# Kernel tuning notes

Hardware: AMD Instinct MI355X
Metric: run time of the kernel (lower is better)

The kernel has to match this reference:

```python
import jax, jax.numpy as jnp
import numpy as np

B, S, D_IN, D_SRC, D_OUT = 128, 2048, 1024, 1024, 1024
W = 64                      # window_size
WL = 2 * W + 1              # window_length
STD_SQ = (W / 2.0) ** 2
EPS = 1e-14


def setup_inputs() -> dict:
    key = jax.random.key(0)
    ks = jax.random.split(key, 8)
    inp = jax.random.normal(ks[0], (B, D_IN), dtype=jnp.float32)
    source_hids = jax.random.normal(ks[1], (S, B, D_SRC), dtype=jnp.float32)
    # per-sample valid lengths; must satisfy L <= S - WL so the dynamic window stays in-bounds
    lengths = jax.random.randint(ks[2], (B,), 1024, S - WL + 1)
    encoder_padding_mask = jnp.arange(S)[:, None] >= lengths[None, :]  # [S, B], True = pad
    d_half = (D_IN + 1) // 2
    u = lambda k, shape, a: jax.random.uniform(k, shape, jnp.float32, -a, a)
    Wi = u(ks[3], (D_SRC, D_IN), 0.1)             # input_proj (no bias)
    Wo = u(ks[4], (D_OUT, D_IN + D_SRC), 0.1)     # output_proj (no bias)
    b1_bound = 1.0 / np.sqrt(D_IN)
    W1 = u(ks[5], (d_half, D_IN), b1_bound); b1 = u(ks[5], (d_half,), b1_bound)
    b2_bound = 1.0 / np.sqrt(d_half)
    W2 = u(ks[6], (1, d_half), b2_bound); b2 = u(ks[6], (1,), b2_bound)
    return {"input": inp, "source_hids": source_hids,
            "encoder_padding_mask": encoder_padding_mask,
            "Wi": Wi, "Wo": Wo, "W1": W1, "b1": b1, "W2": W2, "b2": b2}


def reference(input, source_hids, encoder_padding_mask, Wi, Wo, W1, b1, W2, b2):
    lengths = jnp.sum(~encoder_padding_mask, axis=0).astype(jnp.float32)  # [B]
    x = input @ Wi.T                                                      # [B, D_SRC]
    # predicted window center p = W + L * sigmoid(fc2(tanh(fc1(x))))
    p_sig = jax.nn.sigmoid(jnp.tanh(x @ W1.T + b1) @ W2.T + b2)[:, 0]     # [B]
    p = W + lengths * p_sig                                               # [B]
    window_start = jnp.round(p - W).astype(jnp.int32)                     # [B]
    positions = window_start[:, None].astype(jnp.float32) + jnp.arange(WL, dtype=jnp.float32)  # [B, WL]
    # per-sample dynamic window gather from [B, S, D]
    src_bt = jnp.transpose(source_hids, (1, 0, 2))
    selection = jax.vmap(
        lambda s, st: jax.lax.dynamic_slice(s, (st, 0), (WL, s.shape[1]))
    )(src_bt, window_start)                                               # [B, WL, D_SRC]
    gaussian = jnp.exp(-(positions - p[:, None]) ** 2 / (2.0 * STD_SQ))   # [B, WL]
    score = jnp.einsum('bd,bwd->bw', x, selection)                        # [B, WL]
    # valid absolute positions are [W, L + W); outside -> epsilon (matches torch loop)
    valid = (positions >= W) & (positions < lengths[:, None] + W)
    score = jnp.where(valid, score, EPS)
    a = jax.nn.softmax(score, axis=1) * gaussian                          # [B, WL]
    c = jnp.einsum('bw,bwd->bd', a, selection)                            # [B, D_SRC]
    out = jnp.tanh(jnp.concatenate((c, input), axis=1) @ Wo.T)            # [B, D_OUT]
    return out, a, window_start, window_start + WL
```

## Files before the change

kernel.cpp:

```cpp
#include <hip/hip_runtime.h>
#include <math.h>

#define BB   128
#define SS   2048
#define DIN  1024
#define DSRC 1024
#define DOUT 1024
#define WW   64
#define WLEN 129
#define HH   512
#define WCH  17
#define GW   136

#define OFF_WSI   0
#define OFF_P     512
#define OFF_LEN   1024
#define OFF_GTAB  4096
#define OFF_XP    73728
#define OFF_X32   4268032
#define OFF_Z1P   4792320
#define OFF_C32   6889472
#define OFF_CPART 7413760
#define OFF_MPART 11608064
#define OFF_LPART 11612160
#define OFF_SPART 11616256
#define OFF_OP    11685888
#define WS_NEED   15880192

#define DO_A    (BB*DOUT)
#define DO_WS   (DO_A + BB*WLEN)
#define DO_WE   (DO_WS + BB)

template<int NTOT, int KRANGE, bool F64OUT>
__device__ __forceinline__ void gemm16(const int gblk, const int t,
    const float* __restrict__ A, const int lda,
    const float* __restrict__ Wt, const int ldw,
    void* __restrict__ outp, float* __restrict__ alds )
{
    constexpr int NJB = NTOT / 16;
    const int jb = gblk % NJB;
    const int ks = gblk / NJB;
    const int lane = t & 63;
    const int wvid = __builtin_amdgcn_readfirstlane(t >> 6);
    const int j0 = jb * 16 + wvid * 2;
    const int k0 = ks * KRANGE;

    double dac[2][2];
    dac[0][0] = 0.0; dac[0][1] = 0.0; dac[1][0] = 0.0; dac[1][1] = 0.0;

    const float* wbase = Wt + (size_t)j0 * ldw;

    for (int kc = 0; kc < KRANGE; kc += 64) {
        const int kg = k0 + kc;
        __syncthreads();
        #pragma unroll
        for (int q = 0; q < 4; ++q) {
            const int f4 = t + 512 * q;
            const int bb = f4 >> 4, c4 = f4 & 15;
            const float4 v = *reinterpret_cast<const float4*>(A + (size_t)bb * lda + kg + c4 * 4);
            alds[(c4*4+0)*130 + bb] = v.x;
            alds[(c4*4+1)*130 + bb] = v.y;
            alds[(c4*4+2)*130 + bb] = v.z;
            alds[(c4*4+3)*130 + bb] = v.w;
        }
        __syncthreads();
        const float* wr = wbase + kg;
        #pragma unroll
        for (int kk16 = 0; kk16 < 64; kk16 += 16) {
            float fa[2][2];
            fa[0][0] = 0.f; fa[0][1] = 0.f; fa[1][0] = 0.f; fa[1][1] = 0.f;
            #pragma unroll
            for (int kk = 0; kk < 16; ++kk) {
                const int k = kk16 + kk;
                const float2 av = *reinterpret_cast<const float2*>(&alds[k*130 + 2*lane]);
                #pragma unroll
                for (int jj = 0; jj < 2; ++jj) {
                    const float wvv = wr[jj*ldw + k];
                    fa[jj][0] = fmaf(wvv, av.x, fa[jj][0]);
                    fa[jj][1] = fmaf(wvv, av.y, fa[jj][1]);
                }
            }
            #pragma unroll
            for (int jj = 0; jj < 2; ++jj) {
                dac[jj][0] += (double)fa[jj][0];
                dac[jj][1] += (double)fa[jj][1];
            }
        }
    }
    #pragma unroll
    for (int i = 0; i < 2; ++i) {
        const int b = 2*lane + i;
        const size_t base = ((size_t)ks * BB + b) * NTOT + j0;
        if constexpr (F64OUT) {
            double* o = (double*)outp;
            o[base + 0] = dac[0][i];
            o[base + 1] = dac[1][i];
        } else {
            float* o = (float*)outp;
            o[base + 0] = (float)dac[0][i];
            o[base + 1] = (float)dac[1][i];
        }
    }
}

__global__ __launch_bounds__(512)
void k_combo(const float* __restrict__ input, const float* __restrict__ Wi,
             const float* __restrict__ Wo, const unsigned char* __restrict__ mask,
             double* __restrict__ xp, float* __restrict__ op4, int* __restrict__ lengths)
{
    __shared__ __align__(16) float alds[64*130];
    const int blk = blockIdx.x, t = threadIdx.x;
    if (blk < 256) {
        gemm16<1024, 256, true>(blk, t, input, DIN, Wi, DIN, xp, alds);
    } else if (blk < 512) {
        gemm16<1024, 256, false>(blk - 256, t, input, DIN, Wo + 1024, DIN + DSRC, op4, alds);
    } else {
        const int b = blk - 512;
        const bool is_u8 = (mask[(size_t)SS*BB - 1] != 0);
        int cnt = 0;
        if (is_u8) {
            #pragma unroll
            for (int q = 0; q < 4; ++q)
                cnt += (mask[(size_t)(t + 512*q)*BB + b] != 0) ? 1 : 0;
        } else {
            const int* m32 = (const int*)mask;
            #pragma unroll
            for (int q = 0; q < 4; ++q)
                cnt += (m32[(size_t)(t + 512*q)*BB + b] != 0) ? 1 : 0;
        }
        int* red = (int*)alds;
        red[t] = cnt;
        __syncthreads();
        for (int st = 256; st >= 1; st >>= 1) {
            if (t < st) red[t] += red[t + st];
            __syncthreads();
        }
        if (t == 0) lengths[b] = SS - red[0];
    }
}

__global__ __launch_bounds__(512)
void k_xred(const double* __restrict__ xp, float* __restrict__ x32)
{
    const int i = blockIdx.x * 512 + threadIdx.x;
    double s = 0.0;
    #pragma unroll
    for (int ks = 0; ks < 4; ++ks) s += xp[(size_t)ks * (BB*DSRC) + i];
    x32[i] = (float)s;
}

__global__ __launch_bounds__(512)
void k_fc1(const float* __restrict__ x32, const float* __restrict__ W1, double* __restrict__ z1p)
{
    __shared__ __align__(16) float alds[64*130];
    gemm16<512, 256, true>(blockIdx.x, threadIdx.x, x32, DSRC, W1, DIN, z1p, alds);
}

__global__ __launch_bounds__(64)
void k_fc2(const double* __restrict__ z1p, const float* __restrict__ b1,
           const float* __restrict__ W2f, const float* __restrict__ b2,
           const int* __restrict__ lengths, int* __restrict__ wsi,
           float* __restrict__ pbuf, float* __restrict__ gtab, float* __restrict__ dout)
{
    const int b = blockIdx.x, lane = threadIdx.x;
    double part = 0.0;
    #pragma unroll
    for (int q = 0; q < 8; ++q) {
        const int h = lane + 64*q;
        double z = 0.0;
        #pragma unroll
        for (int ks = 0; ks < 4; ++ks) z += z1p[((size_t)ks*BB + b)*HH + h];
        z += (double)b1[h];
        part += tanh(z) * (double)W2f[h];
    }
    #pragma unroll
    for (int off = 32; off >= 1; off >>= 1) part += __shfl_xor(part, off);
    const double z2  = part + (double)b2[0];
    const double sig = 1.0 / (1.0 + exp(-z2));
    const double wsf = (double)lengths[b] * sig;
    int W0 = (int)rint(wsf);
    if (W0 < 0) W0 = 0;
    if (W0 > SS - WLEN) W0 = SS - WLEN;
    const float pf = (float)(wsf + 64.0);
    if (lane == 0) {
        wsi[b]  = W0;
        pbuf[b] = pf;
        dout[DO_WS + b] = (float)W0;
        dout[DO_WE + b] = (float)(W0 + WLEN);
    }
    #pragma unroll
    for (int q = 0; q < 3; ++q) {
        const int w = lane + 64*q;
        if (w < GW) {
            float g = 0.f;
            if (w < WLEN) {
                const float d = (float)(W0 + w) - pf;
                g = expf(d*d * (-1.0f/2048.0f));
            }
            gtab[b*GW + w] = g;
        }
    }
}

__global__ __launch_bounds__(256)
void k_score(const float* __restrict__ x32, const float* __restrict__ src,
             const int* __restrict__ wsi, const float* __restrict__ pbuf,
             const int* __restrict__ lengths, const float* __restrict__ gtab,
             float* __restrict__ cpart, float* __restrict__ mpart,
             float* __restrict__ lpart, float* __restrict__ spart)
{
    const int wc = blockIdx.x, b = blockIdx.y;
    const int t = threadIdx.x, lane = t & 63, wv = t >> 6;
    const int   w0 = wsi[b];
    const int   L  = lengths[b];

    const float4 x4 = *reinterpret_cast<const float4*>(x32 + b*DSRC + 4*t);

    float4 sel[WCH];
    #pragma unroll
    for (int i = 0; i < WCH; ++i) {
        const int w = wc*WCH + i;
        if (w < WLEN) {
            const size_t off = ((size_t)(w0 + w) * BB + b) * DSRC + 4*t;
            sel[i] = *reinterpret_cast<const float4*>(src + off);
        } else sel[i] = make_float4(0.f, 0.f, 0.f, 0.f);
    }

    float w_[32];
    #pragma unroll
    for (int i = 0; i < WCH; ++i)
        w_[i] = fmaf(x4.x, sel[i].x, fmaf(x4.y, sel[i].y, fmaf(x4.z, sel[i].z, x4.w * sel[i].w)));
    #pragma unroll
    for (int i = WCH; i < 32; ++i) w_[i] = 0.f;

    #pragma unroll
    for (int k = 0; k < 5; ++k) {
        const int dist = 1 << k;
        const bool hi = (lane >> k) & 1;
        const int n2 = 32 >> (k + 1);
        #pragma unroll
        for (int i = 0; i < n2; ++i) {
            const float keep = hi ? w_[2*i+1] : w_[2*i];
            const float send = hi ? w_[2*i]   : w_[2*i+1];
            w_[i] = keep + __shfl_xor(send, dist);
        }
    }
    const float tot = w_[0] + __shfl_xor(w_[0], 32);

    __shared__ float red[WCH][4];
    __shared__ float s_sh[WCH];
    if (lane < WCH) red[lane][wv] = tot;
    __syncthreads();
    if (t < WCH) {
        const int w = wc*WCH + t;
        float s;
        if (w < WLEN) {
            const float sum = red[t][0] + red[t][1] + red[t][2] + red[t][3];
            const int pos = w0 + w;
            s = (pos >= WW && pos < L + WW) ? sum : 1e-14f;
        } else s = -INFINITY;
        s_sh[t] = s;
    }
    __syncthreads();

    float sv[WCH];
    #pragma unroll
    for (int i = 0; i < WCH; ++i) sv[i] = s_sh[i];
    float m_loc = -INFINITY;
    #pragma unroll
    for (int i = 0; i < WCH; ++i) m_loc = fmaxf(m_loc, sv[i]);
    float l_loc = 0.f;
    float4 c = make_float4(0.f, 0.f, 0.f, 0.f);
    #pragma unroll
    for (int i = 0; i < WCH; ++i) {
        const float e = expf(sv[i] - m_loc);
        l_loc += e;
        const float g = gtab[b*GW + wc*WCH + i];
        const float wt = e * g;
        c.x = fmaf(wt, sel[i].x, c.x);
        c.y = fmaf(wt, sel[i].y, c.y);
        c.z = fmaf(wt, sel[i].z, c.z);
        c.w = fmaf(wt, sel[i].w, c.w);
    }
    *reinterpret_cast<float4*>(cpart + ((size_t)(b*8 + wc))*DSRC + 4*t) = c;
    if (t == 0) { mpart[b*8 + wc] = m_loc; lpart[b*8 + wc] = l_loc; }
    if (t < WCH) spart[(b*8 + wc)*WCH + t] = s_sh[t];
}

__global__ __launch_bounds__(256)
void k_merge(const float* __restrict__ cpart, const float* __restrict__ mpart,
             const float* __restrict__ lpart, const float* __restrict__ spart,
             const float* __restrict__ gtab, float* __restrict__ c32,
             float* __restrict__ dout)
{
    const int b = blockIdx.x, t = threadIdx.x;
    __shared__ float mv[8], lv[8];
    if (t < 8) { mv[t] = mpart[b*8 + t]; lv[t] = lpart[b*8 + t]; }
    __syncthreads();
    float m = -INFINITY;
    #pragma unroll
    for (int i = 0; i < 8; ++i) m = fmaxf(m, mv[i]);
    float l = 0.f;
    float fac[8];
    #pragma unroll
    for (int i = 0; i < 8; ++i) { fac[i] = expf(mv[i] - m); l = fmaf(lv[i], fac[i], l); }
    const float inv = 1.0f / l;

    float4 c = make_float4(0.f, 0.f, 0.f, 0.f);
    #pragma unroll
    for (int i = 0; i < 8; ++i) {
        const float4 cp = *reinterpret_cast<const float4*>(cpart + ((size_t)(b*8 + i))*DSRC + 4*t);
        c.x = fmaf(cp.x, fac[i], c.x);
        c.y = fmaf(cp.y, fac[i], c.y);
        c.z = fmaf(cp.z, fac[i], c.z);
        c.w = fmaf(cp.w, fac[i], c.w);
    }
    c.x *= inv; c.y *= inv; c.z *= inv; c.w *= inv;
    *reinterpret_cast<float4*>(c32 + (size_t)b*DSRC + 4*t) = c;

    if (t < WLEN) {
        const int wc = t / WCH, i = t % WCH;
        const float s = spart[(b*8 + wc)*WCH + i];
        const float g = gtab[b*GW + t];
        dout[DO_A + b*WLEN + t] = expf(s - m) * inv * g;
    }
}

__global__ __launch_bounds__(512)
void k_gemm2c(const float* __restrict__ c32, const float* __restrict__ Wo, float* __restrict__ op)
{
    __shared__ __align__(16) float alds[64*130];
    gemm16<1024, 256, false>(blockIdx.x, threadIdx.x, c32, DSRC, Wo, DIN + DSRC, op, alds);
}

__global__ __launch_bounds__(512)
void k_outred(const float* __restrict__ op, float* __restrict__ dout)
{
    const int i = blockIdx.x * 512 + threadIdx.x;
    float s = 0.f;
    #pragma unroll
    for (int ks = 0; ks < 8; ++ks) s += op[(size_t)ks * (BB*DOUT) + i];
    dout[i] = tanhf(s);
}

extern "C" void kernel_launch(void* const* d_in, const int* in_sizes, int n_in,
                              void* d_out, int out_size, void* d_ws, size_t ws_size,
                              hipStream_t stream)
{
    const float* input = (const float*)d_in[0];
    const float* src   = (const float*)d_in[1];
    const unsigned char* mask = (const unsigned char*)d_in[2];
    const float* Wi = (const float*)d_in[3];
    const float* Wo = (const float*)d_in[4];
    const float* W1 = (const float*)d_in[5];
    const float* b1 = (const float*)d_in[6];
    const float* W2 = (const float*)d_in[7];
    const float* b2 = (const float*)d_in[8];
    float* out = (float*)d_out;

    if (ws_size < (size_t)WS_NEED) return;

    char* ws = (char*)d_ws;
    int*    wsi     = (int*)   (ws + OFF_WSI);
    float*  pbuf    = (float*) (ws + OFF_P);
    int*    lengths = (int*)   (ws + OFF_LEN);
    float*  gtab    = (float*) (ws + OFF_GTAB);
    double* xp      = (double*)(ws + OFF_XP);
    float*  x32     = (float*) (ws + OFF_X32);
    double* z1p     = (double*)(ws + OFF_Z1P);
    float*  c32     = (float*) (ws + OFF_C32);
    float*  cpart   = (float*) (ws + OFF_CPART);
    float*  mpart   = (float*) (ws + OFF_MPART);
    float*  lpart   = (float*) (ws + OFF_LPART);
    float*  spart   = (float*) (ws + OFF_SPART);
    float*  op      = (float*) (ws + OFF_OP);

    k_combo<<<640, 512, 0, stream>>>(input, Wi, Wo, mask, xp, op + 4*(size_t)BB*DOUT, lengths);
    k_xred<<<256, 512, 0, stream>>>(xp, x32);
    k_fc1<<<128, 512, 0, stream>>>(x32, W1, z1p);
    k_fc2<<<128, 64, 0, stream>>>(z1p, b1, W2, b2, lengths, wsi, pbuf, gtab, out);
    k_score<<<dim3(8,128), 256, 0, stream>>>(x32, src, wsi, pbuf, lengths, gtab,
                                             cpart, mpart, lpart, spart);
    k_merge<<<128, 256, 0, stream>>>(cpart, mpart, lpart, spart, gtab, c32, out);
    k_gemm2c<<<256, 512, 0, stream>>>(c32, Wo, op);
    k_outred<<<256, 512, 0, stream>>>(op, out);
}
```

Baseline: 75.55 us.

## Fuse fc2 into score kernel and fold output reduction into final GEMM

Removes the separate fc2 kernel. Each score block now recomputes the window start and center for its batch row from z1p, and the Gaussian weights are computed inline instead of read from a table. The split-K output GEMM plus reduction kernel is replaced by a single full-K GEMM over the c half of Wo, which also adds the precomputed input-half partials from k_combo and applies tanh. This cuts two kernel launches and the intermediate traffic, in exchange for redundant fc2 work across the 8 score blocks per row and fewer, longer GEMM blocks (128 blocks of 256 threads) with less parallelism.

```diff
diff --git a/kernel.cpp b/kernel.cpp
--- a/kernel.cpp
+++ b/kernel.cpp
@@ -10,22 +10,20 @@
 #define WLEN 129
 #define HH   512
 #define WCH  17
-#define GW   136
 
 #define OFF_WSI   0
 #define OFF_P     512
 #define OFF_LEN   1024
-#define OFF_GTAB  4096
-#define OFF_XP    73728
-#define OFF_X32   4268032
-#define OFF_Z1P   4792320
-#define OFF_C32   6889472
-#define OFF_CPART 7413760
-#define OFF_MPART 11608064
-#define OFF_LPART 11612160
-#define OFF_SPART 11616256
-#define OFF_OP    11685888
-#define WS_NEED   15880192
+#define OFF_XP    4096
+#define OFF_X32   4198400
+#define OFF_Z1P   4722688
+#define OFF_C32   6819840
+#define OFF_CPART 7344128
+#define OFF_MPART 11538432
+#define OFF_LPART 11542528
+#define OFF_SPART 11546624
+#define OFF_OP4   11616256
+#define WS_NEED   13713408
 
 #define DO_A    (BB*DOUT)
 #define DO_WS   (DO_A + BB*WLEN)
@@ -156,63 +154,64 @@
     gemm16<512, 256, true>(blockIdx.x, threadIdx.x, x32, DSRC, W1, DIN, z1p, alds);
 }
 
-__global__ __launch_bounds__(64)
-void k_fc2(const double* __restrict__ z1p, const float* __restrict__ b1,
-           const float* __restrict__ W2f, const float* __restrict__ b2,
-           const int* __restrict__ lengths, int* __restrict__ wsi,
-           float* __restrict__ pbuf, float* __restrict__ gtab, float* __restrict__ dout)
-{
-    const int b = blockIdx.x, lane = threadIdx.x;
-    double part = 0.0;
-    #pragma unroll
-    for (int q = 0; q < 8; ++q) {
-        const int h = lane + 64*q;
-        double z = 0.0;
-        #pragma unroll
-        for (int ks = 0; ks < 4; ++ks) z += z1p[((size_t)ks*BB + b)*HH + h];
-        z += (double)b1[h];
-        part += tanh(z) * (double)W2f[h];
-    }
-    #pragma unroll
-    for (int off = 32; off >= 1; off >>= 1) part += __shfl_xor(part, off);
-    const double z2  = part + (double)b2[0];
-    const double sig = 1.0 / (1.0 + exp(-z2));
-    const double wsf = (double)lengths[b] * sig;
-    int W0 = (int)rint(wsf);
-    if (W0 < 0) W0 = 0;
-    if (W0 > SS - WLEN) W0 = SS - WLEN;
-    const float pf = (float)(wsf + 64.0);
-    if (lane == 0) {
-        wsi[b]  = W0;
-        pbuf[b] = pf;
-        dout[DO_WS + b] = (float)W0;
-        dout[DO_WE + b] = (float)(W0 + WLEN);
-    }
-    #pragma unroll
-    for (int q = 0; q < 3; ++q) {
-        const int w = lane + 64*q;
-        if (w < GW) {
-            float g = 0.f;
-            if (w < WLEN) {
-                const float d = (float)(W0 + w) - pf;
-                g = expf(d*d * (-1.0f/2048.0f));
-            }
-            gtab[b*GW + w] = g;
-        }
-    }
-}
-
 __global__ __launch_bounds__(256)
 void k_score(const float* __restrict__ x32, const float* __restrict__ src,
-             const int* __restrict__ wsi, const float* __restrict__ pbuf,
-             const int* __restrict__ lengths, const float* __restrict__ gtab,
+             const double* __restrict__ z1p, const float* __restrict__ b1,
+             const float* __restrict__ W2f, const float* __restrict__ b2,
+             const int* __restrict__ lengths,
+             int* __restrict__ wsi, float* __restrict__ pbuf,
              float* __restrict__ cpart, float* __restrict__ mpart,
-             float* __restrict__ lpart, float* __restrict__ spart)
+             float* __restrict__ lpart, float* __restrict__ spart,
+             float* __restrict__ out)
 {
     const int wc = blockIdx.x, b = blockIdx.y;
     const int t = threadIdx.x, lane = t & 63, wv = t >> 6;
-    const int   w0 = wsi[b];
-    const int   L  = lengths[b];
+
+    __shared__ double dred[256];
+    __shared__ float  red[WCH][4];
+    __shared__ float  s_sh[WCH];
+    __shared__ int    W0sh;
+    __shared__ float  psh;
+
+    const int L = lengths[b];
+
+    {
+        double part = 0.0;
+        #pragma unroll
+        for (int hh = 0; hh < 2; ++hh) {
+            const int h = t + 256*hh;
+            double z = 0.0;
+            #pragma unroll
+            for (int ks2 = 0; ks2 < 4; ++ks2) z += z1p[((size_t)ks2*BB + b)*HH + h];
+            z += (double)b1[h];
+            part += tanh(z) * (double)W2f[h];
+        }
+        dred[t] = part;
+        __syncthreads();
+        for (int st = 128; st >= 1; st >>= 1) {
+            if (t < st) dred[t] += dred[t + st];
+            __syncthreads();
+        }
+        if (t == 0) {
+            const double z2  = dred[0] + (double)b2[0];
+            const double sig = 1.0 / (1.0 + exp(-z2));
+            const double wsf = (double)L * sig;
+            int W0 = (int)rint(wsf);
+            if (W0 < 0) W0 = 0;
+            if (W0 > SS - WLEN) W0 = SS - WLEN;
+            W0sh = W0;
+            psh  = (float)(wsf + 64.0);
+            if (wc == 0) {
+                wsi[b]  = W0;
+                pbuf[b] = (float)(wsf + 64.0);
+                out[DO_WS + b] = (float)W0;
+                out[DO_WE + b] = (float)(W0 + WLEN);
+            }
+        }
+        __syncthreads();
+    }
+    const int   w0 = W0sh;
+    const float p  = psh;
 
     const float4 x4 = *reinterpret_cast<const float4*>(x32 + b*DSRC + 4*t);
 
@@ -247,8 +246,6 @@
     }
     const float tot = w_[0] + __shfl_xor(w_[0], 32);
 
-    __shared__ float red[WCH][4];
-    __shared__ float s_sh[WCH];
     if (lane < WCH) red[lane][wv] = tot;
     __syncthreads();
     if (t < WCH) {
@@ -275,7 +272,9 @@
     for (int i = 0; i < WCH; ++i) {
         const float e = expf(sv[i] - m_loc);
         l_loc += e;
-        const float g = gtab[b*GW + wc*WCH + i];
+        const int w = wc*WCH + i;
+        const float d = (float)(w0 + w) - p;
+        const float g = expf(d*d * (-1.0f/2048.0f));
         const float wt = e * g;
         c.x = fmaf(wt, sel[i].x, c.x);
         c.y = fmaf(wt, sel[i].y, c.y);
@@ -290,8 +289,8 @@
 __global__ __launch_bounds__(256)
 void k_merge(const float* __restrict__ cpart, const float* __restrict__ mpart,
              const float* __restrict__ lpart, const float* __restrict__ spart,
-             const float* __restrict__ gtab, float* __restrict__ c32,
-             float* __restrict__ dout)
+             const int* __restrict__ wsi, const float* __restrict__ pbuf,
+             float* __restrict__ c32, float* __restrict__ dout)
 {
     const int b = blockIdx.x, t = threadIdx.x;
     __shared__ float mv[8], lv[8];
@@ -321,26 +320,89 @@
     if (t < WLEN) {
         const int wc = t / WCH, i = t % WCH;
         const float s = spart[(b*8 + wc)*WCH + i];
-        const float g = gtab[b*GW + t];
+        const float d = (float)(wsi[b] + t) - pbuf[b];
+        const float g = expf(d*d * (-1.0f/2048.0f));
         dout[DO_A + b*WLEN + t] = expf(s - m) * inv * g;
     }
 }
 
-__global__ __launch_bounds__(512)
-void k_gemm2c(const float* __restrict__ c32, const float* __restrict__ Wo, float* __restrict__ op)
+__global__ __launch_bounds__(256)
+void k_gemm2cf(const float* __restrict__ c32, const float* __restrict__ Wo,
+               const float* __restrict__ op4, float* __restrict__ out)
 {
     __shared__ __align__(16) float alds[64*130];
-    gemm16<1024, 256, false>(blockIdx.x, threadIdx.x, c32, DSRC, Wo, DIN + DSRC, op, alds);
-}
-
-__global__ __launch_bounds__(512)
-void k_outred(const float* __restrict__ op, float* __restrict__ dout)
-{
-    const int i = blockIdx.x * 512 + threadIdx.x;
-    float s = 0.f;
-    #pragma unroll
-    for (int ks = 0; ks < 8; ++ks) s += op[(size_t)ks * (BB*DOUT) + i];
-    dout[i] = tanhf(s);
+    const int jb = blockIdx.x;
+    const int t = threadIdx.x, lane = t & 63;
+    const int wvid = __builtin_amdgcn_readfirstlane(t >> 6);
+    const int j0 = jb * 8 + wvid * 2;
+    const float* wbase = Wo + (size_t)j0 * (DIN + DSRC);
+
+    double dac[2][2];
+    dac[0][0] = 0.0; dac[0][1] = 0.0; dac[1][0] = 0.0; dac[1][1] = 0.0;
+
+    float4 pf[8];
+    #pragma unroll
+    for (int q = 0; q < 8; ++q) {
+        const int f4 = t + 256*q;
+        const int bb = f4 >> 4, c4 = f4 & 15;
+        pf[q] = *reinterpret_cast<const float4*>(c32 + (size_t)bb*DSRC + c4*4);
+    }
+    for (int c = 0; c < 16; ++c) {
+        __syncthreads();
+        #pragma unroll
+        for (int q = 0; q < 8; ++q) {
+            const int f4 = t + 256*q;
+            const int bb = f4 >> 4, c4 = f4 & 15;
+            alds[(c4*4+0)*130 + bb] = pf[q].x;
+            alds[(c4*4+1)*130 + bb] = pf[q].y;
+            alds[(c4*4+2)*130 + bb] = pf[q].z;
+            alds[(c4*4+3)*130 + bb] = pf[q].w;
+        }
+        __syncthreads();
+        if (c + 1 < 16) {
+            #pragma unroll
+            for (int q = 0; q < 8; ++q) {
+                const int f4 = t + 256*q;
+                const int bb = f4 >> 4, c4 = f4 & 15;
+                pf[q] = *reinterpret_cast<const float4*>(c32 + (size_t)bb*DSRC + (c+1)*64 + c4*4);
+            }
+        }
+        const float* wr = wbase + c*64;
+        #pragma unroll
+        for (int kk16 = 0; kk16 < 64; kk16 += 16) {
+            float fa[2][2];
+            fa[0][0] = 0.f; fa[0][1] = 0.f; fa[1][0] = 0.f; fa[1][1] = 0.f;
+            #pragma unroll
+            for (int kk = 0; kk < 16; ++kk) {
+                const int k = kk16 + kk;
+                const float2 av = *reinterpret_cast<const float2*>(&alds[k*130 + 2*lane]);
+                #pragma unroll
+                for (int jj = 0; jj < 2; ++jj) {
+                    const float wvv = wr[(size_t)jj*(DIN+DSRC) + k];
+                    fa[jj][0] = fmaf(wvv, av.x, fa[jj][0]);
+                    fa[jj][1] = fmaf(wvv, av.y, fa[jj][1]);
+                }
+            }
+            #pragma unroll
+            for (int jj = 0; jj < 2; ++jj) {
+                dac[jj][0] += (double)fa[jj][0];
+                dac[jj][1] += (double)fa[jj][1];
+            }
+        }
+    }
+    #pragma unroll
+    for (int i = 0; i < 2; ++i) {
+        const int b = 2*lane + i;
+        #pragma unroll
+        for (int jj = 0; jj < 2; ++jj) {
+            const int j = j0 + jj;
+            float s = (float)dac[jj][i];
+            #pragma unroll
+            for (int ks2 = 0; ks2 < 4; ++ks2)
+                s += op4[((size_t)ks2*BB + b)*DOUT + j];
+            out[(size_t)b*DOUT + j] = tanhf(s);
+        }
+    }
 }
 
 extern "C" void kernel_launch(void* const* d_in, const int* in_sizes, int n_in,
@@ -364,7 +426,6 @@
     int*    wsi     = (int*)   (ws + OFF_WSI);
     float*  pbuf    = (float*) (ws + OFF_P);
     int*    lengths = (int*)   (ws + OFF_LEN);
-    float*  gtab    = (float*) (ws + OFF_GTAB);
     double* xp      = (double*)(ws + OFF_XP);
     float*  x32     = (float*) (ws + OFF_X32);
     double* z1p     = (double*)(ws + OFF_Z1P);
@@ -373,15 +434,13 @@
     float*  mpart   = (float*) (ws + OFF_MPART);
     float*  lpart   = (float*) (ws + OFF_LPART);
     float*  spart   = (float*) (ws + OFF_SPART);
-    float*  op      = (float*) (ws + OFF_OP);
-
-    k_combo<<<640, 512, 0, stream>>>(input, Wi, Wo, mask, xp, op + 4*(size_t)BB*DOUT, lengths);
+    float*  op4     = (float*) (ws + OFF_OP4);
+
+    k_combo<<<640, 512, 0, stream>>>(input, Wi, Wo, mask, xp, op4, lengths);
     k_xred<<<256, 512, 0, stream>>>(xp, x32);
     k_fc1<<<128, 512, 0, stream>>>(x32, W1, z1p);
-    k_fc2<<<128, 64, 0, stream>>>(z1p, b1, W2, b2, lengths, wsi, pbuf, gtab, out);
-    k_score<<<dim3(8,128), 256, 0, stream>>>(x32, src, wsi, pbuf, lengths, gtab,
-                                             cpart, mpart, lpart, spart);
-    k_merge<<<128, 256, 0, stream>>>(cpart, mpart, lpart, spart, gtab, c32, out);
-    k_gemm2c<<<256, 512, 0, stream>>>(c32, Wo, op);
-    k_outred<<<256, 512, 0, stream>>>(op, out);
-}
+    k_score<<<dim3(8,128), 256, 0, stream>>>(x32, src, z1p, b1, W2, b2, lengths,
+                                             wsi, pbuf, cpart, mpart, lpart, spart, out);
+    k_merge<<<128, 256, 0, stream>>>(cpart, mpart, lpart, spart, wsi, pbuf, c32, out);
+    k_gemm2cf<<<128, 256, 0, stream>>>(c32, Wo, op4, out);
+}
```

Measured after the change: 110.5 us. +46.3%, slower.

## Fuse x split-K reduction into fc1 and score kernels, drop gaussian table

Applied to the files above, without the earlier changes.

Removes the separate k_xred kernel by folding the 4-way double split-K reduction of x into both the fc1 GEMM (now a custom 64-block kernel with 32 outputs per block) and the score kernel. The gaussian table is no longer precomputed in k_fc2; it is recomputed inline in k_score and k_merge from the window start and center. This cuts two launches and some intermediate buffers, at the cost of reading the double partials redundantly and fewer blocks for fc1.

```diff
diff --git a/kernel.cpp b/kernel.cpp
--- a/kernel.cpp
+++ b/kernel.cpp
@@ -10,22 +10,19 @@
 #define WLEN 129
 #define HH   512
 #define WCH  17
-#define GW   136
 
 #define OFF_WSI   0
 #define OFF_P     512
 #define OFF_LEN   1024
-#define OFF_GTAB  4096
-#define OFF_XP    73728
-#define OFF_X32   4268032
-#define OFF_Z1P   4792320
-#define OFF_C32   6889472
-#define OFF_CPART 7413760
-#define OFF_MPART 11608064
-#define OFF_LPART 11612160
-#define OFF_SPART 11616256
-#define OFF_OP    11685888
-#define WS_NEED   15880192
+#define OFF_XP    4096
+#define OFF_Z1P   4198400
+#define OFF_C32   6295552
+#define OFF_CPART 6819840
+#define OFF_MPART 11014144
+#define OFF_LPART 11018240
+#define OFF_SPART 11022336
+#define OFF_OP    11091968
+#define WS_NEED   15286272
 
 #define DO_A    (BB*DOUT)
 #define DO_WS   (DO_A + BB*WLEN)
@@ -140,27 +137,83 @@
 }
 
 __global__ __launch_bounds__(512)
-void k_xred(const double* __restrict__ xp, float* __restrict__ x32)
-{
-    const int i = blockIdx.x * 512 + threadIdx.x;
-    double s = 0.0;
-    #pragma unroll
-    for (int ks = 0; ks < 4; ++ks) s += xp[(size_t)ks * (BB*DSRC) + i];
-    x32[i] = (float)s;
-}
-
-__global__ __launch_bounds__(512)
-void k_fc1(const float* __restrict__ x32, const float* __restrict__ W1, double* __restrict__ z1p)
+void k_fc1x(const double* __restrict__ xp, const float* __restrict__ W1, double* __restrict__ z1p)
 {
     __shared__ __align__(16) float alds[64*130];
-    gemm16<512, 256, true>(blockIdx.x, threadIdx.x, x32, DSRC, W1, DIN, z1p, alds);
+    const int blk = blockIdx.x, t = threadIdx.x;
+    const int jb = blk & 15;
+    const int ks = blk >> 4;
+    const int lane = t & 63;
+    const int wvid = __builtin_amdgcn_readfirstlane(t >> 6);
+    const int j0 = jb * 32 + wvid * 4;
+    const int k0 = ks * 256;
+
+    double dac[4][2];
+    #pragma unroll
+    for (int jj = 0; jj < 4; ++jj) { dac[jj][0] = 0.0; dac[jj][1] = 0.0; }
+
+    const float* wbase = W1 + (size_t)j0 * DIN;
+
+    for (int kc = 0; kc < 256; kc += 64) {
+        const int kg = k0 + kc;
+        __syncthreads();
+        #pragma unroll
+        for (int q = 0; q < 4; ++q) {
+            const int f4 = t + 512 * q;
+            const int bb = f4 >> 4, c4 = f4 & 15;
+            const double* base = xp + (size_t)bb * DSRC + kg + c4 * 4;
+            double s0 = 0.0, s1 = 0.0, s2 = 0.0, s3 = 0.0;
+            #pragma unroll
+            for (int ks2 = 0; ks2 < 4; ++ks2) {
+                const double* p2 = base + (size_t)ks2 * (BB*DSRC);
+                const double2 a = *reinterpret_cast<const double2*>(p2);
+                const double2 c = *reinterpret_cast<const double2*>(p2 + 2);
+                s0 += a.x; s1 += a.y; s2 += c.x; s3 += c.y;
+            }
+            alds[(c4*4+0)*130 + bb] = (float)s0;
+            alds[(c4*4+1)*130 + bb] = (float)s1;
+            alds[(c4*4+2)*130 + bb] = (float)s2;
+            alds[(c4*4+3)*130 + bb] = (float)s3;
+        }
+        __syncthreads();
+        const float* wr = wbase + kg;
+        #pragma unroll
+        for (int kk16 = 0; kk16 < 64; kk16 += 16) {
+            float fa[4][2];
+            #pragma unroll
+            for (int jj = 0; jj < 4; ++jj) { fa[jj][0] = 0.f; fa[jj][1] = 0.f; }
+            #pragma unroll
+            for (int kk = 0; kk < 16; ++kk) {
+                const int k = kk16 + kk;
+                const float2 av = *reinterpret_cast<const float2*>(&alds[k*130 + 2*lane]);
+                #pragma unroll
+                for (int jj = 0; jj < 4; ++jj) {
+                    const float wvv = wr[jj*DIN + k];
+                    fa[jj][0] = fmaf(wvv, av.x, fa[jj][0]);
+                    fa[jj][1] = fmaf(wvv, av.y, fa[jj][1]);
+                }
+            }
+            #pragma unroll
+            for (int jj = 0; jj < 4; ++jj) {
+                dac[jj][0] += (double)fa[jj][0];
+                dac[jj][1] += (double)fa[jj][1];
+            }
+        }
+    }
+    #pragma unroll
+    for (int i = 0; i < 2; ++i) {
+        const int b = 2*lane + i;
+        const size_t base = ((size_t)ks * BB + b) * HH + j0;
+        #pragma unroll
+        for (int jj = 0; jj < 4; ++jj) z1p[base + jj] = dac[jj][i];
+    }
 }
 
 __global__ __launch_bounds__(64)
 void k_fc2(const double* __restrict__ z1p, const float* __restrict__ b1,
            const float* __restrict__ W2f, const float* __restrict__ b2,
            const int* __restrict__ lengths, int* __restrict__ wsi,
-           float* __restrict__ pbuf, float* __restrict__ gtab, float* __restrict__ dout)
+           float* __restrict__ pbuf, float* __restrict__ dout)
 {
     const int b = blockIdx.x, lane = threadIdx.x;
     double part = 0.0;
@@ -175,46 +228,46 @@
     }
     #pragma unroll
     for (int off = 32; off >= 1; off >>= 1) part += __shfl_xor(part, off);
-    const double z2  = part + (double)b2[0];
-    const double sig = 1.0 / (1.0 + exp(-z2));
-    const double wsf = (double)lengths[b] * sig;
-    int W0 = (int)rint(wsf);
-    if (W0 < 0) W0 = 0;
-    if (W0 > SS - WLEN) W0 = SS - WLEN;
-    const float pf = (float)(wsf + 64.0);
     if (lane == 0) {
+        const double z2  = part + (double)b2[0];
+        const double sig = 1.0 / (1.0 + exp(-z2));
+        const double wsf = (double)lengths[b] * sig;
+        int W0 = (int)rint(wsf);
+        if (W0 < 0) W0 = 0;
+        if (W0 > SS - WLEN) W0 = SS - WLEN;
         wsi[b]  = W0;
-        pbuf[b] = pf;
+        pbuf[b] = (float)(wsf + 64.0);
         dout[DO_WS + b] = (float)W0;
         dout[DO_WE + b] = (float)(W0 + WLEN);
     }
-    #pragma unroll
-    for (int q = 0; q < 3; ++q) {
-        const int w = lane + 64*q;
-        if (w < GW) {
-            float g = 0.f;
-            if (w < WLEN) {
-                const float d = (float)(W0 + w) - pf;
-                g = expf(d*d * (-1.0f/2048.0f));
-            }
-            gtab[b*GW + w] = g;
-        }
-    }
 }
 
 __global__ __launch_bounds__(256)
-void k_score(const float* __restrict__ x32, const float* __restrict__ src,
+void k_score(const double* __restrict__ xp, const float* __restrict__ src,
              const int* __restrict__ wsi, const float* __restrict__ pbuf,
-             const int* __restrict__ lengths, const float* __restrict__ gtab,
+             const int* __restrict__ lengths,
              float* __restrict__ cpart, float* __restrict__ mpart,
              float* __restrict__ lpart, float* __restrict__ spart)
 {
     const int wc = blockIdx.x, b = blockIdx.y;
     const int t = threadIdx.x, lane = t & 63, wv = t >> 6;
     const int   w0 = wsi[b];
+    const float p  = pbuf[b];
     const int   L  = lengths[b];
 
-    const float4 x4 = *reinterpret_cast<const float4*>(x32 + b*DSRC + 4*t);
+    float4 x4;
+    {
+        const double* base = xp + (size_t)b * DSRC + 4 * t;
+        double s0 = 0.0, s1 = 0.0, s2 = 0.0, s3 = 0.0;
+        #pragma unroll
+        for (int ks2 = 0; ks2 < 4; ++ks2) {
+            const double* p2 = base + (size_t)ks2 * (BB*DSRC);
+            const double2 a = *reinterpret_cast<const double2*>(p2);
+            const double2 c = *reinterpret_cast<const double2*>(p2 + 2);
+            s0 += a.x; s1 += a.y; s2 += c.x; s3 += c.y;
+        }
+        x4 = make_float4((float)s0, (float)s1, (float)s2, (float)s3);
+    }
 
     float4 sel[WCH];
     #pragma unroll
@@ -275,7 +328,9 @@
     for (int i = 0; i < WCH; ++i) {
         const float e = expf(sv[i] - m_loc);
         l_loc += e;
-        const float g = gtab[b*GW + wc*WCH + i];
+        const int w = wc*WCH + i;
+        const float d = (float)(w0 + w) - p;
+        const float g = expf(d*d * (-1.0f/2048.0f));
         const float wt = e * g;
         c.x = fmaf(wt, sel[i].x, c.x);
         c.y = fmaf(wt, sel[i].y, c.y);
@@ -290,8 +345,8 @@
 __global__ __launch_bounds__(256)
 void k_merge(const float* __restrict__ cpart, const float* __restrict__ mpart,
              const float* __restrict__ lpart, const float* __restrict__ spart,
-             const float* __restrict__ gtab, float* __restrict__ c32,
-             float* __restrict__ dout)
+             const int* __restrict__ wsi, const float* __restrict__ pbuf,
+             float* __restrict__ c32, float* __restrict__ dout)
 {
     const int b = blockIdx.x, t = threadIdx.x;
     __shared__ float mv[8], lv[8];
@@ -321,7 +376,8 @@
     if (t < WLEN) {
         const int wc = t / WCH, i = t % WCH;
         const float s = spart[(b*8 + wc)*WCH + i];
-        const float g = gtab[b*GW + t];
+        const float d = (float)(wsi[b] + t) - pbuf[b];
+        const float g = expf(d*d * (-1.0f/2048.0f));
         dout[DO_A + b*WLEN + t] = expf(s - m) * inv * g;
     }
 }
@@ -364,9 +420,7 @@
     int*    wsi     = (int*)   (ws + OFF_WSI);
     float*  pbuf    = (float*) (ws + OFF_P);
     int*    lengths = (int*)   (ws + OFF_LEN);
-    float*  gtab    = (float*) (ws + OFF_GTAB);
     double* xp      = (double*)(ws + OFF_XP);
-    float*  x32     = (float*) (ws + OFF_X32);
     double* z1p     = (double*)(ws + OFF_Z1P);
     float*  c32     = (float*) (ws + OFF_C32);
     float*  cpart   = (float*) (ws + OFF_CPART);
@@ -376,12 +430,11 @@
     float*  op      = (float*) (ws + OFF_OP);
 
     k_combo<<<640, 512, 0, stream>>>(input, Wi, Wo, mask, xp, op + 4*(size_t)BB*DOUT, lengths);
-    k_xred<<<256, 512, 0, stream>>>(xp, x32);
-    k_fc1<<<128, 512, 0, stream>>>(x32, W1, z1p);
-    k_fc2<<<128, 64, 0, stream>>>(z1p, b1, W2, b2, lengths, wsi, pbuf, gtab, out);
-    k_score<<<dim3(8,128), 256, 0, stream>>>(x32, src, wsi, pbuf, lengths, gtab,
+    k_fc1x<<<64, 512, 0, stream>>>(xp, W1, z1p);
+    k_fc2<<<128, 64, 0, stream>>>(z1p, b1, W2, b2, lengths, wsi, pbuf, out);
+    k_score<<<dim3(8,128), 256, 0, stream>>>(xp, src, wsi, pbuf, lengths,
                                              cpart, mpart, lpart, spart);
-    k_merge<<<128, 256, 0, stream>>>(cpart, mpart, lpart, spart, gtab, c32, out);
+    k_merge<<<128, 256, 0, stream>>>(cpart, mpart, lpart, spart, wsi, pbuf, c32, out);
     k_gemm2c<<<256, 512, 0, stream>>>(c32, Wo, op);
     k_outred<<<256, 512, 0, stream>>>(op, out);
 }
```

Result: slower. 95.01 us (+25.8%).

## Fuse softmax partial merge into output GEMM and merge epilogue kernels

Applied to the files above, without the earlier changes.

Removes the separate k_merge kernel. Each GEMM block now recombines the eight per-chunk context partials (cpart) with log-sum-exp factors while staging its A tile into shared memory, so the c32 intermediate is no longer needed. The attention-weight output and the tanh reduction are folded into one epilogue kernel. This saves one launch and the c32 round trip. In exchange, the cpart merge work is repeated across the 64 column blocks (8x more A-side reads per block), and every block recomputes the factors for all 128 batch rows.

```diff
diff --git a/kernel.cpp b/kernel.cpp
--- a/kernel.cpp
+++ b/kernel.cpp
@@ -19,7 +19,6 @@
 #define OFF_XP    73728
 #define OFF_X32   4268032
 #define OFF_Z1P   4792320
-#define OFF_C32   6889472
 #define OFF_CPART 7413760
 #define OFF_MPART 11608064
 #define OFF_LPART 11612160
@@ -287,60 +286,130 @@
     if (t < WCH) spart[(b*8 + wc)*WCH + t] = s_sh[t];
 }
 
-__global__ __launch_bounds__(256)
-void k_merge(const float* __restrict__ cpart, const float* __restrict__ mpart,
-             const float* __restrict__ lpart, const float* __restrict__ spart,
-             const float* __restrict__ gtab, float* __restrict__ c32,
-             float* __restrict__ dout)
-{
-    const int b = blockIdx.x, t = threadIdx.x;
-    __shared__ float mv[8], lv[8];
-    if (t < 8) { mv[t] = mpart[b*8 + t]; lv[t] = lpart[b*8 + t]; }
-    __syncthreads();
-    float m = -INFINITY;
-    #pragma unroll
-    for (int i = 0; i < 8; ++i) m = fmaxf(m, mv[i]);
-    float l = 0.f;
-    float fac[8];
-    #pragma unroll
-    for (int i = 0; i < 8; ++i) { fac[i] = expf(mv[i] - m); l = fmaf(lv[i], fac[i], l); }
-    const float inv = 1.0f / l;
-
-    float4 c = make_float4(0.f, 0.f, 0.f, 0.f);
-    #pragma unroll
-    for (int i = 0; i < 8; ++i) {
-        const float4 cp = *reinterpret_cast<const float4*>(cpart + ((size_t)(b*8 + i))*DSRC + 4*t);
-        c.x = fmaf(cp.x, fac[i], c.x);
-        c.y = fmaf(cp.y, fac[i], c.y);
-        c.z = fmaf(cp.z, fac[i], c.z);
-        c.w = fmaf(cp.w, fac[i], c.w);
-    }
-    c.x *= inv; c.y *= inv; c.z *= inv; c.w *= inv;
-    *reinterpret_cast<float4*>(c32 + (size_t)b*DSRC + 4*t) = c;
-
-    if (t < WLEN) {
-        const int wc = t / WCH, i = t % WCH;
-        const float s = spart[(b*8 + wc)*WCH + i];
-        const float g = gtab[b*GW + t];
-        dout[DO_A + b*WLEN + t] = expf(s - m) * inv * g;
-    }
-}
-
 __global__ __launch_bounds__(512)
-void k_gemm2c(const float* __restrict__ c32, const float* __restrict__ Wo, float* __restrict__ op)
+void k_gemm2cm(const float* __restrict__ cpart, const float* __restrict__ mpart,
+               const float* __restrict__ lpart, const float* __restrict__ Wo,
+               float* __restrict__ op)
 {
     __shared__ __align__(16) float alds[64*130];
-    gemm16<1024, 256, false>(blockIdx.x, threadIdx.x, c32, DSRC, Wo, DIN + DSRC, op, alds);
+    __shared__ float fac_s[128][8];
+    __shared__ float inv_s[128];
+
+    const int blk = blockIdx.x, t = threadIdx.x;
+    const int jb = blk & 63;
+    const int ks = blk >> 6;
+    const int lane = t & 63;
+    const int wvid = __builtin_amdgcn_readfirstlane(t >> 6);
+    const int j0 = jb * 16 + wvid * 2;
+    const int k0 = ks * 256;
+
+    if (t < 128) {
+        float mv[8], lv[8];
+        #pragma unroll
+        for (int i = 0; i < 8; ++i) { mv[i] = mpart[t*8 + i]; lv[i] = lpart[t*8 + i]; }
+        float m = -INFINITY;
+        #pragma unroll
+        for (int i = 0; i < 8; ++i) m = fmaxf(m, mv[i]);
+        float l = 0.f;
+        float fc[8];
+        #pragma unroll
+        for (int i = 0; i < 8; ++i) { fc[i] = expf(mv[i] - m); l = fmaf(lv[i], fc[i], l); }
+        inv_s[t] = 1.0f / l;
+        #pragma unroll
+        for (int i = 0; i < 8; ++i) fac_s[t][i] = fc[i];
+    }
+
+    double dac[2][2];
+    dac[0][0] = 0.0; dac[0][1] = 0.0; dac[1][0] = 0.0; dac[1][1] = 0.0;
+
+    const float* wbase = Wo + (size_t)j0 * (DIN + DSRC);
+
+    for (int kc = 0; kc < 256; kc += 64) {
+        const int kg = k0 + kc;
+        __syncthreads();
+        #pragma unroll
+        for (int q = 0; q < 4; ++q) {
+            const int f4 = t + 512 * q;
+            const int bb = f4 >> 4, c4 = f4 & 15;
+            const float* cb = cpart + ((size_t)bb * 8) * DSRC + kg + c4 * 4;
+            float4 s = make_float4(0.f, 0.f, 0.f, 0.f);
+            #pragma unroll
+            for (int i = 0; i < 8; ++i) {
+                const float4 cp = *reinterpret_cast<const float4*>(cb + (size_t)i * DSRC);
+                const float f = fac_s[bb][i];
+                s.x = fmaf(cp.x, f, s.x);
+                s.y = fmaf(cp.y, f, s.y);
+                s.z = fmaf(cp.z, f, s.z);
+                s.w = fmaf(cp.w, f, s.w);
+            }
+            const float iv = inv_s[bb];
+            alds[(c4*4+0)*130 + bb] = s.x * iv;
+            alds[(c4*4+1)*130 + bb] = s.y * iv;
+            alds[(c4*4+2)*130 + bb] = s.z * iv;
+            alds[(c4*4+3)*130 + bb] = s.w * iv;
+        }
+        __syncthreads();
+        const float* wr = wbase + kg;
+        #pragma unroll
+        for (int kk16 = 0; kk16 < 64; kk16 += 16) {
+            float fa[2][2];
+            fa[0][0] = 0.f; fa[0][1] = 0.f; fa[1][0] = 0.f; fa[1][1] = 0.f;
+            #pragma unroll
+            for (int kk = 0; kk < 16; ++kk) {
+                const int k = kk16 + kk;
+                const float2 av = *reinterpret_cast<const float2*>(&alds[k*130 + 2*lane]);
+                #pragma unroll
+                for (int jj = 0; jj < 2; ++jj) {
+                    const float wvv = wr[jj*(DIN+DSRC) + k];
+                    fa[jj][0] = fmaf(wvv, av.x, fa[jj][0]);
+                    fa[jj][1] = fmaf(wvv, av.y, fa[jj][1]);
+                }
+            }
+            #pragma unroll
+            for (int jj = 0; jj < 2; ++jj) {
+                dac[jj][0] += (double)fa[jj][0];
+                dac[jj][1] += (double)fa[jj][1];
+            }
+        }
+    }
+    #pragma unroll
+    for (int i = 0; i < 2; ++i) {
+        const int b = 2*lane + i;
+        const size_t base = ((size_t)ks * BB + b) * DOUT + j0;
+        op[base + 0] = (float)dac[0][i];
+        op[base + 1] = (float)dac[1][i];
+    }
 }
 
 __global__ __launch_bounds__(512)
-void k_outred(const float* __restrict__ op, float* __restrict__ dout)
-{
-    const int i = blockIdx.x * 512 + threadIdx.x;
-    float s = 0.f;
-    #pragma unroll
-    for (int ks = 0; ks < 8; ++ks) s += op[(size_t)ks * (BB*DOUT) + i];
-    dout[i] = tanhf(s);
+void k_epi(const float* __restrict__ op, const float* __restrict__ mpart,
+           const float* __restrict__ lpart, const float* __restrict__ spart,
+           const float* __restrict__ gtab, float* __restrict__ out)
+{
+    const int idx = blockIdx.x * 512 + threadIdx.x;
+    if (idx < BB*DOUT) {
+        float s = 0.f;
+        #pragma unroll
+        for (int ks = 0; ks < 8; ++ks) s += op[(size_t)ks * (BB*DOUT) + idx];
+        out[idx] = tanhf(s);
+    } else if (idx < BB*DOUT + BB*WLEN) {
+        const int j = idx - BB*DOUT;
+        const int b = j / WLEN, w = j - b*WLEN;
+        float mv[8], lv[8];
+        #pragma unroll
+        for (int i = 0; i < 8; ++i) { mv[i] = mpart[b*8 + i]; lv[i] = lpart[b*8 + i]; }
+        float m = -INFINITY;
+        #pragma unroll
+        for (int i = 0; i < 8; ++i) m = fmaxf(m, mv[i]);
+        float l = 0.f;
+        #pragma unroll
+        for (int i = 0; i < 8; ++i) { const float f = expf(mv[i] - m); l = fmaf(lv[i], f, l); }
+        const float inv = 1.0f / l;
+        const int wc = w / WCH, i2 = w - wc*WCH;
+        const float s = spart[(b*8 + wc)*WCH + i2];
+        const float g = gtab[b*GW + w];
+        out[DO_A + j] = expf(s - m) * inv * g;
+    }
 }
 
 extern "C" void kernel_launch(void* const* d_in, const int* in_sizes, int n_in,
@@ -368,7 +437,6 @@
     double* xp      = (double*)(ws + OFF_XP);
     float*  x32     = (float*) (ws + OFF_X32);
     double* z1p     = (double*)(ws + OFF_Z1P);
-    float*  c32     = (float*) (ws + OFF_C32);
     float*  cpart   = (float*) (ws + OFF_CPART);
     float*  mpart   = (float*) (ws + OFF_MPART);
     float*  lpart   = (float*) (ws + OFF_LPART);
@@ -381,7 +449,6 @@
     k_fc2<<<128, 64, 0, stream>>>(z1p, b1, W2, b2, lengths, wsi, pbuf, gtab, out);
     k_score<<<dim3(8,128), 256, 0, stream>>>(x32, src, wsi, pbuf, lengths, gtab,
                                              cpart, mpart, lpart, spart);
-    k_merge<<<128, 256, 0, stream>>>(cpart, mpart, lpart, spart, gtab, c32, out);
-    k_gemm2c<<<256, 512, 0, stream>>>(c32, Wo, op);
-    k_outred<<<256, 512, 0, stream>>>(op, out);
-}
+    k_gemm2cm<<<256, 512, 0, stream>>>(cpart, mpart, lpart, Wo, op);
+    k_epi<<<289, 512, 0, stream>>>(op, mpart, lpart, spart, gtab, out);
+}
```

Result: slower. 88.42 us (+17.0%).
